# Kernel tuning notes

Measured on AMD Instinct MI355X. Metric: run time of the kernel, lower is better.

The kernel has to match this reference:

```python
import jax, jax.numpy as jnp
import numpy as np

B = 16
PATCH_NUM = 32      # L of inter branch
PATCH_SIZE = 128    # L of intra branch
WIN_SIZE = PATCH_NUM * PATCH_SIZE  # 4096
H = 8
E = 64


def setup_inputs() -> dict:
    key = jax.random.key(0)
    ks = jax.random.split(key, 6)
    return {
        "q_inter": jax.random.normal(ks[0], (B, PATCH_NUM, H, E), jnp.float32),
        "k_inter": jax.random.normal(ks[1], (B, PATCH_NUM, H, E), jnp.float32),
        "v_inter": jax.random.normal(ks[2], (B, PATCH_NUM, H, E), jnp.float32),
        "q_intra": jax.random.normal(ks[3], (B, PATCH_SIZE, H, E), jnp.float32),
        "k_intra": jax.random.normal(ks[4], (B, PATCH_SIZE, H, E), jnp.float32),
        "v_intra": jax.random.normal(ks[5], (B, PATCH_SIZE, H, E), jnp.float32),
    }


def _full_attention(q, k, v):
    # q,k,v: [B, L, H, E]; full softmax attention, scale = 1/sqrt(E)
    scale = 1.0 / jnp.sqrt(jnp.asarray(q.shape[-1], q.dtype))
    score = jnp.einsum('blhe,bshe->bhls', q, k) * scale
    att = jax.nn.softmax(score, axis=-1)  # dropout is identity in eval mode
    return jnp.einsum('bhls,bshd->blhd', att, v)


def reference(q_inter, k_inter, v_inter, q_intra, k_intra, v_intra):
    V_inter = _full_attention(q_inter, k_inter, v_inter)  # [B, patch_num, H, E]
    V_intra = _full_attention(q_intra, k_intra, v_intra)  # [B, patch_size, H, E]
    # einops repeat 'b pn h d -> b (pn ps) h d': each patch repeated ps times
    V_inter_up = jnp.repeat(V_inter, PATCH_SIZE, axis=1)  # [B, win_size, H, E]
    # einops repeat 'b ps h d -> b (ps pn) h d': each position repeated pn times
    V_intra_up = jnp.repeat(V_intra, PATCH_NUM, axis=1)   # [B, win_size, H, E]
    return V_inter_up + V_intra_up
```

## Files before the change

### kernel.cpp

```cpp
#include <hip/hip_runtime.h>


#define NH 8
#define NE 64
#define ROWSTRIDE 512

typedef float  vf4 __attribute__((ext_vector_type(4)));
typedef short  v8s __attribute__((ext_vector_type(8)));

__device__ __forceinline__ float dot4(const float4 a, const float4 b) {
    return a.x * b.x + a.y * b.y + a.z * b.z + a.w * b.w;
}

__device__ __forceinline__ unsigned short f2bf(float f) {
    unsigned int u = __float_as_uint(f);
    u += 0x7fff + ((u >> 16) & 1);
    return (unsigned short)(u >> 16);
}

#define SMEM_BYTES 51328
#define OFF_QB  18432
#define OFF_R2  23040
#define OFF_IV  31744
#define OFF_P   40448
#define OFF_IO  49152

__global__ __launch_bounds__(256, 2) void attn_mfma(
    const float* __restrict__ qI, const float* __restrict__ kI, const float* __restrict__ vI,
    const float* __restrict__ qT, const float* __restrict__ kT, const float* __restrict__ vT,
    float* __restrict__ wsSum)
{
    __shared__ __align__(16) char smem[SMEM_BYTES];

    const int tid  = threadIdx.x;
    const int bid  = blockIdx.x;
    const int tile = bid & 3;
    const int h    = (bid >> 2) & 7;
    const int b    = bid >> 5;
    const int r0   = tile * 32;
    const int pn0  = tile * 8;

    {
        const float* kg = kI + ((size_t)b * 32 * NH + h) * NE;
        const float* vg = vI + ((size_t)b * 32 * NH + h) * NE;
        float* dK = (float*)(smem + OFF_R2);
        float* dV = (float*)(smem + OFF_IV);
        for (int idx = tid; idx < 32 * 16; idx += 256) {
            const int row = idx >> 4;
            const int f   = (idx & 15) * 4;
            *(float4*)&dK[row * 68 + f] = *(const float4*)(kg + (size_t)row * ROWSTRIDE + f);
            *(float4*)&dV[row * 64 + f] = *(const float4*)(vg + (size_t)row * ROWSTRIDE + f);
        }
    }
    __syncthreads();

    {
        const float* kgT = kT + ((size_t)b * 128 * NH + h) * NE;
        unsigned short* wKb = (unsigned short*)smem;
        for (int idx = tid; idx < 128 * 16; idx += 256) {
            const int row = idx >> 4;
            const int f   = (idx & 15) * 4;
            const float4 v = *(const float4*)(kgT + (size_t)row * ROWSTRIDE + f);
            ushort4 pk; pk.x = f2bf(v.x); pk.y = f2bf(v.y); pk.z = f2bf(v.z); pk.w = f2bf(v.w);
            *(ushort4*)(wKb + row * 72 + f) = pk;
        }
        const float* qgT = qT + ((size_t)(b * 128 + r0) * NH + h) * NE;
        unsigned short* wQb = (unsigned short*)(smem + OFF_QB);
        for (int idx = tid; idx < 32 * 16; idx += 256) {
            const int row = idx >> 4;
            const int f   = (idx & 15) * 4;
            const float4 v = *(const float4*)(qgT + (size_t)row * ROWSTRIDE + f);
            ushort4 pk; pk.x = f2bf(v.x); pk.y = f2bf(v.y); pk.z = f2bf(v.z); pk.w = f2bf(v.w);
            *(ushort4*)(wQb + row * 72 + f) = pk;
        }
    }

    {
        const int rg = tid >> 5;
        const int ln = tid & 31;
        const float* dK  = (const float*)(smem + OFF_R2);
        const float* dV  = (const float*)(smem + OFF_IV);
        float*       sIO = (float*)(smem + OFF_IO);

        const float* qrow = qI + ((size_t)(b * 32 + pn0 + rg) * NH + h) * NE;
        float s = 0.f;
        #pragma unroll
        for (int e = 0; e < NE; e += 4) {
            const float4 qv = *(const float4*)(qrow + e);
            const float4 kv = *(const float4*)&dK[ln * 68 + e];
            s += dot4(qv, kv);
        }
        s *= 0.125f;
        float m = s;
        #pragma unroll
        for (int msk = 1; msk < 32; msk <<= 1) m = fmaxf(m, __shfl_xor(m, msk));
        const float pe = __expf(s - m);
        float sum = pe;
        #pragma unroll
        for (int msk = 1; msk < 32; msk <<= 1) sum += __shfl_xor(sum, msk);
        const float pn = pe / sum;

        const int hw = tid & 32;
        float o0 = 0.f, o1 = 0.f;
        #pragma unroll 8
        for (int c = 0; c < 32; c++) {
            const float pc = __shfl(pn, hw + c);
            const float2 v = *(const float2*)&dV[c * 64 + ln * 2];
            o0 += pc * v.x;
            o1 += pc * v.y;
        }
        sIO[rg * 68 + ln * 2]     = o0;
        sIO[rg * 68 + ln * 2 + 1] = o1;
    }
    __syncthreads();

    {
        const float* vgT = vT + ((size_t)b * 128 * NH + h) * NE;
        unsigned short* wVb = (unsigned short*)(smem + OFF_R2);
        for (int idx = tid; idx < 128 * 16; idx += 256) {
            const int c = idx >> 4;
            const int f = (idx & 15) * 4;
            const float4 v = *(const float4*)(vgT + (size_t)c * ROWSTRIDE + f);
            const float arr[4] = { v.x, v.y, v.z, v.w };
            #pragma unroll
            for (int i = 0; i < 4; i++) {
                const int j = (c + i) & 3;
                wVb[(f + j) * 136 + c] = f2bf(arr[j]);
            }
        }
    }
    __syncthreads();

    const int lane = tid & 63;
    const int ln15 = lane & 15;
    const int quad = lane >> 4;
    const int w    = tid >> 6;
    const int mt   = w & 1;
    const int ntb  = (w >> 1) * 4;

    vf4 accS[4];
    #pragma unroll
    for (int t = 0; t < 4; t++) accS[t] = (vf4){0.f, 0.f, 0.f, 0.f};
    {
        const unsigned short* sKb = (const unsigned short*)smem;
        const unsigned short* sQb = (const unsigned short*)(smem + OFF_QB);
        #pragma unroll
        for (int kt = 0; kt < 2; kt++) {
            const v8s aQ = *(const v8s*)(sQb + (mt * 16 + ln15) * 72 + kt * 32 + quad * 8);
            #pragma unroll
            for (int t = 0; t < 4; t++) {
                const v8s bK = *(const v8s*)(sKb + ((ntb + t) * 16 + ln15) * 72 + kt * 32 + quad * 8);
                accS[t] = __builtin_amdgcn_mfma_f32_16x16x32_bf16(aQ, bK, accS[t], 0, 0, 0);
            }
        }
    }
    __syncthreads();

    {
        float* sS = (float*)smem;
        #pragma unroll
        for (int t = 0; t < 4; t++)
            #pragma unroll
            for (int reg = 0; reg < 4; reg++)
                sS[(mt * 16 + quad * 4 + reg) * 132 + (ntb + t) * 16 + ln15]
                    = accS[t][reg] * 0.125f;
    }
    __syncthreads();

    {
        const float* sS = (const float*)smem;
        unsigned short* sP = (unsigned short*)(smem + OFF_P);
        const int r   = tid >> 3;
        const int sub = tid & 7;
        float vals[16];
        const float* Srow = sS + r * 132 + sub * 16;
        #pragma unroll
        for (int c4 = 0; c4 < 4; c4++) {
            const float4 v = *(const float4*)(Srow + c4 * 4);
            vals[c4*4+0] = v.x; vals[c4*4+1] = v.y; vals[c4*4+2] = v.z; vals[c4*4+3] = v.w;
        }
        float m = vals[0];
        #pragma unroll
        for (int i = 1; i < 16; i++) m = fmaxf(m, vals[i]);
        #pragma unroll
        for (int msk = 1; msk < 8; msk <<= 1) m = fmaxf(m, __shfl_xor(m, msk));
        float s = 0.f;
        #pragma unroll
        for (int i = 0; i < 16; i++) { vals[i] = __expf(vals[i] - m); s += vals[i]; }
        #pragma unroll
        for (int msk = 1; msk < 8; msk <<= 1) s += __shfl_xor(s, msk);
        const float inv = 1.f / s;
        #pragma unroll
        for (int c4 = 0; c4 < 4; c4++) {
            ushort4 pk;
            pk.x = f2bf(vals[c4*4+0] * inv); pk.y = f2bf(vals[c4*4+1] * inv);
            pk.z = f2bf(vals[c4*4+2] * inv); pk.w = f2bf(vals[c4*4+3] * inv);
            *(ushort4*)(sP + r * 136 + sub * 16 + c4 * 4) = pk;
        }
    }
    __syncthreads();

    {
        const unsigned short* sVb = (const unsigned short*)(smem + OFF_R2);
        const unsigned short* sP  = (const unsigned short*)(smem + OFF_P);
        const float*          sIO = (const float*)(smem + OFF_IO);
        const int neb = (w >> 1) * 2;

        vf4 accO[2];
        accO[0] = (vf4){0.f, 0.f, 0.f, 0.f};
        accO[1] = (vf4){0.f, 0.f, 0.f, 0.f};
        #pragma unroll
        for (int kt = 0; kt < 4; kt++) {
            const v8s aP = *(const v8s*)(sP + (mt * 16 + ln15) * 136 + kt * 32 + quad * 8);
            #pragma unroll
            for (int t = 0; t < 2; t++) {
                const v8s bV = *(const v8s*)(sVb + ((neb + t) * 16 + ln15) * 136 + kt * 32 + quad * 8);
                accO[t] = __builtin_amdgcn_mfma_f32_16x16x32_bf16(aP, bV, accO[t], 0, 0, 0);
            }
        }

        #pragma unroll
        for (int t = 0; t < 2; t++) {
            const int e   = (neb + t) * 16 + ln15;
            const float vin = sIO[(mt * 4 + quad) * 68 + e];
            #pragma unroll
            for (int reg = 0; reg < 4; reg++) {
                const int row = r0 + mt * 16 + quad * 4 + reg;
                wsSum[((size_t)(b * 128 + row) * NH + h) * NE + e] = accO[t][reg] + vin;
            }
        }
    }
}

__global__ __launch_bounds__(256) void duplicate_kernel(
    const float4* __restrict__ ws, float* __restrict__ out)
{
    const int t  = blockIdx.x * 256 + threadIdx.x;
    const int e4 = t & 15;
    const int h  = (t >> 4) & 7;
    const int pi = (t >> 7) & 127;
    const int b  = t >> 14;

    const float4 a = ws[((b * 128 + pi) * NH + h) * 16 + e4];
    vf4 s; s.x = a.x; s.y = a.y; s.z = a.z; s.w = a.w;

    float* o = out + ((((size_t)b * 4096 + pi * 32) * NH + h) * 16 + e4) * 4;
    #pragma unroll
    for (int j = 0; j < 32; j++)
        __builtin_nontemporal_store(s, (vf4*)(o + (size_t)j * ROWSTRIDE));
}

extern "C" void kernel_launch(void* const* d_in, const int* in_sizes, int n_in,
                              void* d_out, int out_size, void* d_ws, size_t ws_size,
                              hipStream_t stream) {
    const float* q_inter = (const float*)d_in[0];
    const float* k_inter = (const float*)d_in[1];
    const float* v_inter = (const float*)d_in[2];
    const float* q_intra = (const float*)d_in[3];
    const float* k_intra = (const float*)d_in[4];
    const float* v_intra = (const float*)d_in[5];
    float* out = (float*)d_out;
    float* ws  = (float*)d_ws;

    attn_mfma<<<512, 256, 0, stream>>>(
        q_inter, k_inter, v_inter, q_intra, k_intra, v_intra, ws);

    duplicate_kernel<<<1024, 256, 0, stream>>>((const float4*)ws, out);
}
```

Measured before the change: 170.9 us.

## Split inter-patch attention into dedicated blocks and add in duplicate kernel

The 32-token inter-patch attention moves into 128 dedicated blocks that each compute all 32 rows for one (batch, head). Previously every intra tile block recomputed its slice and reloaded the inter K/V, four times per (batch, head). The intra blocks drop the inter K/V staging and its sync, which cuts shared memory enough to raise the launch bound to 3 blocks per CU. The duplicate kernel now reads both workspace buffers and does the add, at the cost of one extra small read per thread and a more divergent first kernel.

```diff
diff --git a/kernel.cpp b/kernel.cpp
--- a/kernel.cpp
+++ b/kernel.cpp
@@ -18,109 +18,106 @@
     return (unsigned short)(u >> 16);
 }
 
-#define SMEM_BYTES 51328
+#define SMEM_BYTES 49152
 #define OFF_QB  18432
-#define OFF_R2  23040
-#define OFF_IV  31744
+#define OFF_VB  23040
 #define OFF_P   40448
-#define OFF_IO  49152
-
-__global__ __launch_bounds__(256, 2) void attn_mfma(
+
+__global__ __launch_bounds__(256, 3) void attn_split(
     const float* __restrict__ qI, const float* __restrict__ kI, const float* __restrict__ vI,
     const float* __restrict__ qT, const float* __restrict__ kT, const float* __restrict__ vT,
-    float* __restrict__ wsSum)
+    float* __restrict__ wsT, float* __restrict__ wsI)
 {
     __shared__ __align__(16) char smem[SMEM_BYTES];
-
-    const int tid  = threadIdx.x;
-    const int bid  = blockIdx.x;
-    const int tile = bid & 3;
-    const int h    = (bid >> 2) & 7;
-    const int b    = bid >> 5;
+    const int tid = threadIdx.x;
+    const int bid = blockIdx.x;
+
+    if (bid < 128) {
+        const int b = bid >> 3;
+        const int h = bid & 7;
+        float* dK = (float*)smem;
+        float* dV = (float*)(smem + 8704);
+        {
+            const float* kg = kI + ((size_t)b * 32 * NH + h) * NE;
+            const float* vg = vI + ((size_t)b * 32 * NH + h) * NE;
+            for (int idx = tid; idx < 32 * 16; idx += 256) {
+                const int row = idx >> 4;
+                const int f   = (idx & 15) * 4;
+                *(float4*)&dK[row * 68 + f] = *(const float4*)(kg + (size_t)row * ROWSTRIDE + f);
+                *(float4*)&dV[row * 64 + f] = *(const float4*)(vg + (size_t)row * ROWSTRIDE + f);
+            }
+        }
+        __syncthreads();
+
+        const int rg = tid >> 5;
+        const int ln = tid & 31;
+        const int hw = tid & 32;
+        #pragma unroll
+        for (int it = 0; it < 4; it++) {
+            const int row = it * 8 + rg;
+            const float* qrow = qI + ((size_t)(b * 32 + row) * NH + h) * NE;
+            float s = 0.f;
+            #pragma unroll
+            for (int e = 0; e < NE; e += 4) {
+                const float4 qv = *(const float4*)(qrow + e);
+                const float4 kv = *(const float4*)&dK[ln * 68 + e];
+                s += dot4(qv, kv);
+            }
+            s *= 0.125f;
+            float m = s;
+            #pragma unroll
+            for (int msk = 1; msk < 32; msk <<= 1) m = fmaxf(m, __shfl_xor(m, msk));
+            const float pe = __expf(s - m);
+            float sum = pe;
+            #pragma unroll
+            for (int msk = 1; msk < 32; msk <<= 1) sum += __shfl_xor(sum, msk);
+            const float pn = pe / sum;
+
+            float o0 = 0.f, o1 = 0.f;
+            #pragma unroll 8
+            for (int c = 0; c < 32; c++) {
+                const float pc = __shfl(pn, hw + c);
+                const float2 v = *(const float2*)&dV[c * 64 + ln * 2];
+                o0 += pc * v.x;
+                o1 += pc * v.y;
+            }
+            float2 o2; o2.x = o0; o2.y = o1;
+            *(float2*)(wsI + ((size_t)(b * 32 + row) * NH + h) * NE + ln * 2) = o2;
+        }
+        return;
+    }
+
+    const int ib   = bid - 128;
+    const int tile = ib & 3;
+    const int h    = (ib >> 2) & 7;
+    const int b    = ib >> 5;
     const int r0   = tile * 32;
-    const int pn0  = tile * 8;
-
-    {
-        const float* kg = kI + ((size_t)b * 32 * NH + h) * NE;
-        const float* vg = vI + ((size_t)b * 32 * NH + h) * NE;
-        float* dK = (float*)(smem + OFF_R2);
-        float* dV = (float*)(smem + OFF_IV);
-        for (int idx = tid; idx < 32 * 16; idx += 256) {
-            const int row = idx >> 4;
-            const int f   = (idx & 15) * 4;
-            *(float4*)&dK[row * 68 + f] = *(const float4*)(kg + (size_t)row * ROWSTRIDE + f);
-            *(float4*)&dV[row * 64 + f] = *(const float4*)(vg + (size_t)row * ROWSTRIDE + f);
-        }
-    }
-    __syncthreads();
-
-    {
-        const float* kgT = kT + ((size_t)b * 128 * NH + h) * NE;
+
+    {
+        const float* kg = kT + ((size_t)b * 128 * NH + h) * NE;
         unsigned short* wKb = (unsigned short*)smem;
         for (int idx = tid; idx < 128 * 16; idx += 256) {
             const int row = idx >> 4;
             const int f   = (idx & 15) * 4;
-            const float4 v = *(const float4*)(kgT + (size_t)row * ROWSTRIDE + f);
+            const float4 v = *(const float4*)(kg + (size_t)row * ROWSTRIDE + f);
             ushort4 pk; pk.x = f2bf(v.x); pk.y = f2bf(v.y); pk.z = f2bf(v.z); pk.w = f2bf(v.w);
             *(ushort4*)(wKb + row * 72 + f) = pk;
         }
-        const float* qgT = qT + ((size_t)(b * 128 + r0) * NH + h) * NE;
+        const float* qg = qT + ((size_t)(b * 128 + r0) * NH + h) * NE;
         unsigned short* wQb = (unsigned short*)(smem + OFF_QB);
         for (int idx = tid; idx < 32 * 16; idx += 256) {
             const int row = idx >> 4;
             const int f   = (idx & 15) * 4;
-            const float4 v = *(const float4*)(qgT + (size_t)row * ROWSTRIDE + f);
+            const float4 v = *(const float4*)(qg + (size_t)row * ROWSTRIDE + f);
             ushort4 pk; pk.x = f2bf(v.x); pk.y = f2bf(v.y); pk.z = f2bf(v.z); pk.w = f2bf(v.w);
             *(ushort4*)(wQb + row * 72 + f) = pk;
         }
-    }
-
-    {
-        const int rg = tid >> 5;
-        const int ln = tid & 31;
-        const float* dK  = (const float*)(smem + OFF_R2);
-        const float* dV  = (const float*)(smem + OFF_IV);
-        float*       sIO = (float*)(smem + OFF_IO);
-
-        const float* qrow = qI + ((size_t)(b * 32 + pn0 + rg) * NH + h) * NE;
-        float s = 0.f;
-        #pragma unroll
-        for (int e = 0; e < NE; e += 4) {
-            const float4 qv = *(const float4*)(qrow + e);
-            const float4 kv = *(const float4*)&dK[ln * 68 + e];
-            s += dot4(qv, kv);
-        }
-        s *= 0.125f;
-        float m = s;
-        #pragma unroll
-        for (int msk = 1; msk < 32; msk <<= 1) m = fmaxf(m, __shfl_xor(m, msk));
-        const float pe = __expf(s - m);
-        float sum = pe;
-        #pragma unroll
-        for (int msk = 1; msk < 32; msk <<= 1) sum += __shfl_xor(sum, msk);
-        const float pn = pe / sum;
-
-        const int hw = tid & 32;
-        float o0 = 0.f, o1 = 0.f;
-        #pragma unroll 8
-        for (int c = 0; c < 32; c++) {
-            const float pc = __shfl(pn, hw + c);
-            const float2 v = *(const float2*)&dV[c * 64 + ln * 2];
-            o0 += pc * v.x;
-            o1 += pc * v.y;
-        }
-        sIO[rg * 68 + ln * 2]     = o0;
-        sIO[rg * 68 + ln * 2 + 1] = o1;
-    }
-    __syncthreads();
-
-    {
-        const float* vgT = vT + ((size_t)b * 128 * NH + h) * NE;
-        unsigned short* wVb = (unsigned short*)(smem + OFF_R2);
+        const float* vg = vT + ((size_t)b * 128 * NH + h) * NE;
+        unsigned short* wVb = (unsigned short*)(smem + OFF_VB);
         for (int idx = tid; idx < 128 * 16; idx += 256) {
             const int c = idx >> 4;
             const int f = (idx & 15) * 4;
-            const float4 v = *(const float4*)(vgT + (size_t)c * ROWSTRIDE + f);
+            const float4 v = *(const float4*)(vg + (size_t)c * ROWSTRIDE + f);
             const float arr[4] = { v.x, v.y, v.z, v.w };
             #pragma unroll
             for (int i = 0; i < 4; i++) {
@@ -201,9 +198,8 @@
     __syncthreads();
 
     {
-        const unsigned short* sVb = (const unsigned short*)(smem + OFF_R2);
+        const unsigned short* sVb = (const unsigned short*)(smem + OFF_VB);
         const unsigned short* sP  = (const unsigned short*)(smem + OFF_P);
-        const float*          sIO = (const float*)(smem + OFF_IO);
         const int neb = (w >> 1) * 2;
 
         vf4 accO[2];
@@ -218,22 +214,21 @@
                 accO[t] = __builtin_amdgcn_mfma_f32_16x16x32_bf16(aP, bV, accO[t], 0, 0, 0);
             }
         }
-
         #pragma unroll
         for (int t = 0; t < 2; t++) {
-            const int e   = (neb + t) * 16 + ln15;
-            const float vin = sIO[(mt * 4 + quad) * 68 + e];
+            const int e = (neb + t) * 16 + ln15;
             #pragma unroll
             for (int reg = 0; reg < 4; reg++) {
                 const int row = r0 + mt * 16 + quad * 4 + reg;
-                wsSum[((size_t)(b * 128 + row) * NH + h) * NE + e] = accO[t][reg] + vin;
-            }
-        }
-    }
-}
-
-__global__ __launch_bounds__(256) void duplicate_kernel(
-    const float4* __restrict__ ws, float* __restrict__ out)
+                wsT[((size_t)(b * 128 + row) * NH + h) * NE + e] = accO[t][reg];
+            }
+        }
+    }
+}
+
+__global__ __launch_bounds__(256) void duplicate_add_kernel(
+    const float4* __restrict__ wsT, const float4* __restrict__ wsI,
+    float* __restrict__ out)
 {
     const int t  = blockIdx.x * 256 + threadIdx.x;
     const int e4 = t & 15;
@@ -241,8 +236,9 @@
     const int pi = (t >> 7) & 127;
     const int b  = t >> 14;
 
-    const float4 a = ws[((b * 128 + pi) * NH + h) * 16 + e4];
-    vf4 s; s.x = a.x; s.y = a.y; s.z = a.z; s.w = a.w;
+    const float4 a = wsT[((b * 128 + pi) * NH + h) * 16 + e4];
+    const float4 c = wsI[((b * 32 + (pi >> 2)) * NH + h) * 16 + e4];
+    vf4 s; s.x = a.x + c.x; s.y = a.y + c.y; s.z = a.z + c.z; s.w = a.w + c.w;
 
     float* o = out + ((((size_t)b * 4096 + pi * 32) * NH + h) * 16 + e4) * 4;
     #pragma unroll
@@ -260,10 +256,12 @@
     const float* k_intra = (const float*)d_in[4];
     const float* v_intra = (const float*)d_in[5];
     float* out = (float*)d_out;
-    float* ws  = (float*)d_ws;
-
-    attn_mfma<<<512, 256, 0, stream>>>(
-        q_inter, k_inter, v_inter, q_intra, k_intra, v_intra, ws);
-
-    duplicate_kernel<<<1024, 256, 0, stream>>>((const float4*)ws, out);
-}
+    float* wsT = (float*)d_ws;
+    float* wsI = wsT + (size_t)16 * 128 * NH * NE;
+
+    attn_split<<<640, 256, 0, stream>>>(
+        q_inter, k_inter, v_inter, q_intra, k_intra, v_intra, wsT, wsI);
+
+    duplicate_add_kernel<<<1024, 256, 0, stream>>>(
+        (const float4*)wsT, (const float4*)wsI, out);
+}
```

Measured after the change: 170.2 us. About the same (-0.4%).
